# Kernel optimization log

Hardware: AMD Instinct MI355X
Metric: run time of the kernel (lower is better)

The kernel has to match this reference:

```python
import jax, jax.numpy as jnp
import numpy as np

S, B, D = 2048, 16, 512  # seq_len, batch, dim_in (= value_dim)


def setup_inputs() -> dict:
    key = jax.random.key(0)
    k1, k2, k3 = jax.random.split(key, 3)
    seq = jax.random.normal(k1, (S, B, D), dtype=jnp.float32)
    # torch nn.Linear(dim_in, value_dim): weight [value_dim, dim_in], bias [value_dim]
    bound = 1.0 / np.sqrt(D)
    Wv = jax.random.uniform(k2, (D, D), minval=-bound, maxval=bound, dtype=jnp.float32)
    bv = jax.random.uniform(k3, (D,), minval=-bound, maxval=bound, dtype=jnp.float32)
    return {"seq": seq, "Wv": Wv, "bv": bv}


def reference(seq, Wv, bv):
    # seq: [S, B, D] -> seq_in: [B, S, D]
    seq_in = jnp.transpose(seq, (1, 0, 2))
    # value = tanh(Linear(seq_in)); query = value; keys = seq_in (raw input)
    value = jnp.tanh(jnp.einsum('bsd,vd->bsv', seq_in, Wv) + bv)  # [B, S, Dv]
    # unscaled score matrix value @ value^T -> [B, S, S]
    weights = jnp.einsum('bsv,btv->bst', value, value)
    weights = jax.nn.softmax(weights, axis=-1)
    out = jnp.einsum('bst,btd->bsd', weights, seq_in)  # [B, S, D]
    return jnp.transpose(out, (1, 0, 2))  # [S, B, D]
```

## Files before the change

kernel.cpp:

```cpp
#include <hip/hip_runtime.h>

#define S_LEN 2048
#define BATCH 16
#define DIM   512
#define KVB   64
#define NT    (S_LEN / KVB)

typedef __bf16 bf16x8 __attribute__((ext_vector_type(8)));
typedef float  f32x4  __attribute__((ext_vector_type(4)));
typedef float  f32x16 __attribute__((ext_vector_type(16)));
typedef unsigned int u32x4 __attribute__((ext_vector_type(4)));

static __device__ __forceinline__ unsigned short f2bf(float f) {
    __bf16 h = (__bf16)f;
    return __builtin_bit_cast(unsigned short, h);
}
static __device__ __forceinline__ bf16x8 ld_bf8(const unsigned short* p) {
    u32x4 v = *reinterpret_cast<const u32x4*>(p);
    return __builtin_bit_cast(bf16x8, v);
}
static __device__ __forceinline__ f32x4 mfma16(bf16x8 a, bf16x8 b, f32x4 c) {
    return __builtin_amdgcn_mfma_f32_16x16x32_bf16(a, b, c, 0, 0, 0);
}
static __device__ __forceinline__ f32x16 mfma32(bf16x8 a, bf16x8 b, f32x16 c) {
    return __builtin_amdgcn_mfma_f32_32x32x16_bf16(a, b, c, 0, 0, 0);
}
static __device__ __forceinline__ void gload16(const unsigned short* g, unsigned short* l) {
    __builtin_amdgcn_global_load_lds(
        (const __attribute__((address_space(1))) unsigned int*)g,
        (__attribute__((address_space(3))) unsigned int*)l, 16, 0, 0);
}
#define WAITV(N) do { asm volatile("s_waitcnt vmcnt(" #N ")" ::: "memory"); \
                      __builtin_amdgcn_sched_barrier(0); } while (0)
static __device__ __forceinline__ void waitlg0() {
    asm volatile("s_waitcnt lgkmcnt(0)" ::: "memory");
    __builtin_amdgcn_sched_barrier(0);
}

__global__ void pack_seq(const float* __restrict__ seq, unsigned short* __restrict__ seqb,
                         unsigned short* __restrict__ vt) {
    __shared__ float tile[32][33];
    int b  = blockIdx.z;
    int d0 = blockIdx.y * 32;
    int s0 = blockIdx.x * 32;
    int t  = threadIdx.x;
    {
        int sl = t >> 3, c4 = (t & 7) * 4;
        float4 v = *reinterpret_cast<const float4*>(
            seq + (size_t)(s0 + sl) * (BATCH * DIM) + (size_t)b * DIM + d0 + c4);
        tile[sl][c4 + 0] = v.x; tile[sl][c4 + 1] = v.y;
        tile[sl][c4 + 2] = v.z; tile[sl][c4 + 3] = v.w;
        uint2 r;
        r.x = (unsigned)f2bf(v.x) | ((unsigned)f2bf(v.y) << 16);
        r.y = (unsigned)f2bf(v.z) | ((unsigned)f2bf(v.w) << 16);
        int s = s0 + sl, d = d0 + c4;
        size_t off = ((size_t)(b * 128 + (s >> 4)) * 16 + (d >> 5)) * 512
                     + (s & 15) * 32 + (d & 31);
        *reinterpret_cast<uint2*>(seqb + off) = r;
    }
    __syncthreads();
    {
        int dl = t >> 3, s4 = (t & 7) * 4;
        uint2 r;
        r.x = (unsigned)f2bf(tile[s4 + 0][dl]) | ((unsigned)f2bf(tile[s4 + 1][dl]) << 16);
        r.y = (unsigned)f2bf(tile[s4 + 2][dl]) | ((unsigned)f2bf(tile[s4 + 3][dl]) << 16);
        int d = d0 + dl, s = s0 + s4;
        size_t off = ((size_t)(b * 128 + (s >> 4)) * 16 + (d >> 5)) * 512
                     + (d & 31) * 16 + (s & 15);
        *reinterpret_cast<uint2*>(vt + off) = r;
    }
}

__global__ void pack_vt(const float* __restrict__ seq, unsigned short* __restrict__ vt) {
    __shared__ float tile[32][33];
    int b  = blockIdx.z;
    int d0 = blockIdx.y * 32;
    int s0 = blockIdx.x * 32;
    int t  = threadIdx.x;
    {
        int sl = t >> 3, c4 = (t & 7) * 4;
        float4 v = *reinterpret_cast<const float4*>(
            seq + (size_t)(s0 + sl) * (BATCH * DIM) + (size_t)b * DIM + d0 + c4);
        tile[sl][c4 + 0] = v.x; tile[sl][c4 + 1] = v.y;
        tile[sl][c4 + 2] = v.z; tile[sl][c4 + 3] = v.w;
    }
    __syncthreads();
    {
        int dl = t >> 3, s4 = (t & 7) * 4;
        uint2 r;
        r.x = (unsigned)f2bf(tile[s4 + 0][dl]) | ((unsigned)f2bf(tile[s4 + 1][dl]) << 16);
        r.y = (unsigned)f2bf(tile[s4 + 2][dl]) | ((unsigned)f2bf(tile[s4 + 3][dl]) << 16);
        int d = d0 + dl, s = s0 + s4;
        size_t off = ((size_t)(b * 128 + (s >> 4)) * 16 + (d >> 5)) * 512
                     + (d & 31) * 16 + (s & 15);
        *reinterpret_cast<uint2*>(vt + off) = r;
    }
}

template <bool BF16A>
__global__ void __launch_bounds__(256) gemm_value(
        const float* __restrict__ seq, const unsigned short* __restrict__ seqb,
        const float* __restrict__ wv, const float* __restrict__ bv,
        unsigned short* __restrict__ val) {
    __shared__ unsigned short Asm[64][72];
    __shared__ unsigned short Bsm[64][72];
    int t  = threadIdx.x;
    int rb = blockIdx.x * 64;
    int cb = blockIdx.y * 64;
    int w = t >> 6, l = t & 63;
    int mi = w >> 1, ni = w & 1;
    int l15 = l & 15, lh = l >> 4;
    f32x4 acc[2][2] = {};

    int srow = t >> 2;
    int qc   = (t & 3) * 16;
    int gr = rb + srow;
    int sb = gr >> 11, ss = gr & 2047;
    const float* aSrc = seq + ((size_t)ss * BATCH + sb) * DIM + qc;
    const float* bSrc = wv + (size_t)(cb + srow) * DIM + qc;

    for (int k0 = 0; k0 < DIM; k0 += 64) {
        if (BF16A) {
            int dcol = k0 + qc;
            const unsigned short* p = seqb
                + ((size_t)(sb * 128 + (ss >> 4)) * 16 + (dcol >> 5)) * 512
                + (ss & 15) * 32 + (dcol & 31);
            *reinterpret_cast<u32x4*>(&Asm[srow][qc])     = *reinterpret_cast<const u32x4*>(p);
            *reinterpret_cast<u32x4*>(&Asm[srow][qc + 8]) = *reinterpret_cast<const u32x4*>(p + 8);
        } else {
            unsigned short ar[16];
            #pragma unroll
            for (int j = 0; j < 4; ++j) {
                float4 v = *reinterpret_cast<const float4*>(aSrc + k0 + j * 4);
                ar[j * 4 + 0] = f2bf(v.x); ar[j * 4 + 1] = f2bf(v.y);
                ar[j * 4 + 2] = f2bf(v.z); ar[j * 4 + 3] = f2bf(v.w);
            }
            *reinterpret_cast<u32x4*>(&Asm[srow][qc])     = *reinterpret_cast<u32x4*>(&ar[0]);
            *reinterpret_cast<u32x4*>(&Asm[srow][qc + 8]) = *reinterpret_cast<u32x4*>(&ar[8]);
        }
        {
            unsigned short br[16];
            #pragma unroll
            for (int j = 0; j < 4; ++j) {
                float4 u = *reinterpret_cast<const float4*>(bSrc + k0 + j * 4);
                br[j * 4 + 0] = f2bf(u.x); br[j * 4 + 1] = f2bf(u.y);
                br[j * 4 + 2] = f2bf(u.z); br[j * 4 + 3] = f2bf(u.w);
            }
            *reinterpret_cast<u32x4*>(&Bsm[srow][qc])     = *reinterpret_cast<u32x4*>(&br[0]);
            *reinterpret_cast<u32x4*>(&Bsm[srow][qc + 8]) = *reinterpret_cast<u32x4*>(&br[8]);
        }
        __syncthreads();
        #pragma unroll
        for (int kf = 0; kf < 2; ++kf) {
            bf16x8 af[2], bfm[2];
            #pragma unroll
            for (int i = 0; i < 2; ++i)
                af[i] = ld_bf8(&Asm[mi * 32 + i * 16 + l15][kf * 32 + lh * 8]);
            #pragma unroll
            for (int j = 0; j < 2; ++j)
                bfm[j] = ld_bf8(&Bsm[ni * 32 + j * 16 + l15][kf * 32 + lh * 8]);
            #pragma unroll
            for (int i = 0; i < 2; ++i)
                #pragma unroll
                for (int j = 0; j < 2; ++j)
                    acc[i][j] = mfma16(af[i], bfm[j], acc[i][j]);
        }
        __syncthreads();
    }
    #pragma unroll
    for (int i = 0; i < 2; ++i) {
        #pragma unroll
        for (int j = 0; j < 2; ++j) {
            int gcol = cb + ni * 32 + j * 16 + l15;
            float bias = bv[gcol];
            #pragma unroll
            for (int r = 0; r < 4; ++r) {
                int grow = rb + mi * 32 + i * 16 + lh * 4 + r;
                float x = acc[i][j][r] + bias;
                int b_ = grow >> 11, s_ = grow & 2047;
                size_t off = ((size_t)(b_ * 128 + (s_ >> 4)) * 16 + (gcol >> 5)) * 512
                             + (s_ & 15) * 32 + (gcol & 31);
                val[off] = f2bf(tanhf(x));
            }
        }
    }
}

__global__ void __launch_bounds__(512, 2) attn_fused(
        const unsigned short* __restrict__ val, const unsigned short* __restrict__ vt,
        float* __restrict__ out) {
    extern __shared__ char smem[];
    unsigned short* Kb = (unsigned short*)smem;
    unsigned short* Vb = (unsigned short*)(smem + 65536);
    float*          Sb = (float*)(smem + 131072);
    unsigned short* PS = (unsigned short*)(smem + 148480);
    float* stm = (float*)(smem + 156928);
    float* stl = stm + 64;
    float* sts = stm + 128;

    const int t = threadIdx.x;
    const int w = t >> 6, l = t & 63;
    const int l15 = l & 15, lh = l >> 4;
    const int l31 = l & 31, lh1 = l >> 5;

    int wg  = blockIdx.x;
    int swz = (wg & 7) * 64 + (wg >> 3);
    int b   = swz >> 5;
    int qb  = (swz & 31) * 64;

    const int qi = w & 3, khi = w >> 2;
    const int dq = w;

    const unsigned short* valb = val + (size_t)b * 128 * 16 * 512;
    const unsigned short* vtb  = vt  + (size_t)b * 128 * 16 * 512;

    if (t < 64) { stm[t] = -3.0e38f; stl[t] = 0.0f; }

    bf16x8 qf[16];
    {
        const unsigned short* qp = valb + ((size_t)((qb >> 4) + qi) * 16) * 512
                                   + l15 * 32 + lh * 8;
        #pragma unroll
        for (int ks = 0; ks < 16; ++ks) qf[ks] = ld_bf8(qp + (size_t)ks * 512);
    }
    f32x16 o[4] = {};

    auto dmaK = [&](int kt) {
        #pragma unroll
        for (int i = 0; i < 8; ++i) {
            int idx = i * 8 + w, g = idx >> 4, ks = idx & 15;
            gload16(valb + ((size_t)(kt * 4 + g) * 16 + ks) * 512 + l15 * 32 + lh * 8,
                    Kb + idx * 512);
        }
    };
    auto dmaV = [&](int kt) {
        #pragma unroll
        for (int i = 0; i < 8; ++i) {
            int idx = i * 8 + w, ks = idx >> 4, dt = idx & 15;
            gload16(vtb + ((size_t)(kt * 4 + ks) * 16 + dt) * 512 + l31 * 16 + lh1 * 8,
                    Vb + idx * 512);
        }
    };

    dmaK(0);
    dmaV(0);
    WAITV(0);
    __builtin_amdgcn_s_barrier();

    for (int kt = 0; kt < NT; ++kt) {
        WAITV(8);
        __builtin_amdgcn_s_barrier();
        {
            const unsigned short* kb0 = Kb + (size_t)(2 * khi) * 16 * 512 + l * 8;
            const unsigned short* kb1 = kb0 + 16 * 512;
            f32x4 a0 = {}, a1 = {};
            __builtin_amdgcn_s_setprio(1);
            #pragma unroll
            for (int ks = 0; ks < 16; ++ks) {
                bf16x8 k0 = ld_bf8(kb0 + ks * 512);
                bf16x8 k1 = ld_bf8(kb1 + ks * 512);
                a0 = mfma16(qf[ks], k0, a0);
                a1 = mfma16(qf[ks], k1, a1);
            }
            __builtin_amdgcn_s_setprio(0);
            #pragma unroll
            for (int r = 0; r < 4; ++r) {
                Sb[(qi * 16 + lh * 4 + r) * 68 + khi * 32 + l15]      = a0[r];
                Sb[(qi * 16 + lh * 4 + r) * 68 + khi * 32 + 16 + l15] = a1[r];
            }
        }
        waitlg0();
        __builtin_amdgcn_s_barrier();

        {
            int nk = (kt + 1 < NT) ? kt + 1 : NT - 1;
            dmaK(nk);
        }
        {
            int row = t >> 3, e = t & 7;
            const float* sp = Sb + row * 68 + e * 8;
            f32x4 x0 = *reinterpret_cast<const f32x4*>(sp);
            f32x4 x1 = *reinterpret_cast<const f32x4*>(sp + 4);
            float mt = fmaxf(fmaxf(fmaxf(x0[0], x0[1]), fmaxf(x0[2], x0[3])),
                             fmaxf(fmaxf(x1[0], x1[1]), fmaxf(x1[2], x1[3])));
            #pragma unroll
            for (int m = 1; m <= 4; m <<= 1) mt = fmaxf(mt, __shfl_xor(mt, m, 64));
            float m_old = stm[row];
            float m_new = (mt > m_old + 8.0f) ? mt : m_old;
            float e0 = __expf(x0[0] - m_new), e1 = __expf(x0[1] - m_new);
            float e2 = __expf(x0[2] - m_new), e3 = __expf(x0[3] - m_new);
            float e4 = __expf(x1[0] - m_new), e5 = __expf(x1[1] - m_new);
            float e6 = __expf(x1[2] - m_new), e7 = __expf(x1[3] - m_new);
            float lt = ((e0 + e1) + (e2 + e3)) + ((e4 + e5) + (e6 + e7));
            #pragma unroll
            for (int m = 1; m <= 4; m <<= 1) lt += __shfl_xor(lt, m, 64);
            u32x4 pk;
            pk[0] = (unsigned)f2bf(e0) | ((unsigned)f2bf(e1) << 16);
            pk[1] = (unsigned)f2bf(e2) | ((unsigned)f2bf(e3) << 16);
            pk[2] = (unsigned)f2bf(e4) | ((unsigned)f2bf(e5) << 16);
            pk[3] = (unsigned)f2bf(e6) | ((unsigned)f2bf(e7) << 16);
            int ks = e >> 1, qg = row >> 5;
            unsigned short* pdst = PS + ((qg * 4 + ks) * 512 + ks * 8)
                                   + ((e & 1) * 32 + (row & 31)) * 8;
            *reinterpret_cast<u32x4*>(pdst) = pk;
            if (e == 0) {
                float alpha = (m_new == m_old) ? 1.0f : __expf(m_old - m_new);
                sts[row] = alpha;
                stm[row] = m_new;
                stl[row] = stl[row] * alpha + lt;
            }
        }
        waitlg0();
        WAITV(8);
        __builtin_amdgcn_s_barrier();

        {
            f32x4 al[2][4];
            bool need = false;
            #pragma unroll
            for (int qg = 0; qg < 2; ++qg)
                #pragma unroll
                for (int c = 0; c < 4; ++c) {
                    al[qg][c] = *reinterpret_cast<const f32x4*>(
                        sts + qg * 32 + 4 * lh1 + 8 * c);
                    #pragma unroll
                    for (int j = 0; j < 4; ++j) need = need || (al[qg][c][j] != 1.0f);
                }
            if (__any((int)need)) {
                #pragma unroll
                for (int qg = 0; qg < 2; ++qg)
                    #pragma unroll
                    for (int dtl = 0; dtl < 2; ++dtl)
                        #pragma unroll
                        for (int rr = 0; rr < 16; ++rr)
                            o[qg * 2 + dtl][rr] *= al[qg][rr >> 2][rr & 3];
            }
            __builtin_amdgcn_s_setprio(1);
            #pragma unroll
            for (int ks = 0; ks < 4; ++ks) {
                bf16x8 pa0 = ld_bf8(PS + ((0 + ks) * 512 + ks * 8) + l * 8);
                bf16x8 pa1 = ld_bf8(PS + ((4 + ks) * 512 + ks * 8) + l * 8);
                #pragma unroll
                for (int dtl = 0; dtl < 2; ++dtl) {
                    bf16x8 vf = ld_bf8(Vb + (size_t)(ks * 16 + dq * 2 + dtl) * 512 + l * 8);
                    o[0 + dtl] = mfma32(pa0, vf, o[0 + dtl]);
                    o[2 + dtl] = mfma32(pa1, vf, o[2 + dtl]);
                }
            }
            __builtin_amdgcn_s_setprio(0);
        }
        waitlg0();
        __builtin_amdgcn_s_barrier();
        {
            int nv = (kt + 1 < NT) ? kt + 1 : NT - 1;
            dmaV(nv);
        }
    }

    #pragma unroll
    for (int qg = 0; qg < 2; ++qg) {
        f32x4 li[4];
        #pragma unroll
        for (int c = 0; c < 4; ++c) {
            f32x4 lv = *reinterpret_cast<const f32x4*>(stl + qg * 32 + 4 * lh1 + 8 * c);
            #pragma unroll
            for (int j = 0; j < 4; ++j) li[c][j] = 1.0f / lv[j];
        }
        #pragma unroll
        for (int dtl = 0; dtl < 2; ++dtl) {
            int col = dq * 64 + dtl * 32 + l31;
            #pragma unroll
            for (int rr = 0; rr < 16; ++rr) {
                int cr  = (rr & 3) + 8 * (rr >> 2) + 4 * lh1;
                int row = qb + qg * 32 + cr;
                out[(size_t)row * (BATCH * DIM) + (size_t)b * DIM + col] =
                    o[qg * 2 + dtl][rr] * li[rr >> 2][rr & 3];
            }
        }
    }
}

extern "C" void kernel_launch(void* const* d_in, const int* in_sizes, int n_in,
                              void* d_out, int out_size, void* d_ws, size_t ws_size,
                              hipStream_t stream) {
    const float* seq = (const float*)d_in[0];
    const float* wv  = (const float*)d_in[1];
    const float* bv  = (const float*)d_in[2];
    float* outp = (float*)d_out;

    unsigned short* wsVal  = (unsigned short*)d_ws;
    unsigned short* wsVt   = (unsigned short*)((char*)d_ws + 33554432);
    unsigned short* wsSeqb = (unsigned short*)((char*)d_ws + 67108864);

    bool fused = ws_size >= 100663296ull;
    if (fused) {
        pack_seq<<<dim3(S_LEN / 32, DIM / 32, BATCH), dim3(256), 0, stream>>>(
            seq, wsSeqb, wsVt);
        gemm_value<true><<<dim3(BATCH * S_LEN / 64, DIM / 64), dim3(256), 0, stream>>>(
            seq, wsSeqb, wv, bv, wsVal);
    } else {
        pack_vt<<<dim3(S_LEN / 32, DIM / 32, BATCH), dim3(256), 0, stream>>>(seq, wsVt);
        gemm_value<false><<<dim3(BATCH * S_LEN / 64, DIM / 64), dim3(256), 0, stream>>>(
            seq, nullptr, wv, bv, wsVal);
    }
    attn_fused<<<dim3(512), dim3(512), 157696, stream>>>(wsVal, wsVt, outp);
}
```

Baseline: 296.5 us.

## Store tanh value tensor as FP8 e4m3 and compute QK scores with FP8 MFMA

The value projection output is now written as FP8 e4m3 in a repacked layout instead of bf16. The attention kernel computes scores with 16x16x32 fp8 MFMAs, using two accumulators per tile that are summed afterwards. This halves K/Q bytes loaded and LDS space for K, and the wait count is adjusted for fewer K DMA instructions. The cost is precision: unscaled scores summed over 512 dims feed a softmax, so FP8 rounding of tanh values may shift the attention weights noticeably.

```diff
diff --git a/kernel.cpp b/kernel.cpp
--- a/kernel.cpp
+++ b/kernel.cpp
@@ -1,4 +1,5 @@
 #include <hip/hip_runtime.h>
+#include <hip/hip_fp8.h>
 
 #define S_LEN 2048
 #define BATCH 16
@@ -10,11 +11,16 @@
 typedef float  f32x4  __attribute__((ext_vector_type(4)));
 typedef float  f32x16 __attribute__((ext_vector_type(16)));
 typedef unsigned int u32x4 __attribute__((ext_vector_type(4)));
+typedef long long llx2 __attribute__((ext_vector_type(2)));
 
 static __device__ __forceinline__ unsigned short f2bf(float f) {
     __bf16 h = (__bf16)f;
     return __builtin_bit_cast(unsigned short, h);
 }
+static __device__ __forceinline__ unsigned char f2fp8(float f) {
+    __hip_fp8_e4m3 h(f);
+    return h.__x;
+}
 static __device__ __forceinline__ bf16x8 ld_bf8(const unsigned short* p) {
     u32x4 v = *reinterpret_cast<const u32x4*>(p);
     return __builtin_bit_cast(bf16x8, v);
@@ -22,10 +28,13 @@
 static __device__ __forceinline__ f32x4 mfma16(bf16x8 a, bf16x8 b, f32x4 c) {
     return __builtin_amdgcn_mfma_f32_16x16x32_bf16(a, b, c, 0, 0, 0);
 }
+static __device__ __forceinline__ f32x4 mfma8(long long a, long long b, f32x4 c) {
+    return __builtin_amdgcn_mfma_f32_16x16x32_fp8_fp8(a, b, c, 0, 0, 0);
+}
 static __device__ __forceinline__ f32x16 mfma32(bf16x8 a, bf16x8 b, f32x16 c) {
     return __builtin_amdgcn_mfma_f32_32x32x16_bf16(a, b, c, 0, 0, 0);
 }
-static __device__ __forceinline__ void gload16(const unsigned short* g, unsigned short* l) {
+static __device__ __forceinline__ void gload16(const void* g, void* l) {
     __builtin_amdgcn_global_load_lds(
         (const __attribute__((address_space(1))) unsigned int*)g,
         (__attribute__((address_space(3))) unsigned int*)l, 16, 0, 0);
@@ -101,7 +110,7 @@
 __global__ void __launch_bounds__(256) gemm_value(
         const float* __restrict__ seq, const unsigned short* __restrict__ seqb,
         const float* __restrict__ wv, const float* __restrict__ bv,
-        unsigned short* __restrict__ val) {
+        unsigned char* __restrict__ val8) {
     __shared__ unsigned short Asm[64][72];
     __shared__ unsigned short Bsm[64][72];
     int t  = threadIdx.x;
@@ -173,28 +182,30 @@
         for (int j = 0; j < 2; ++j) {
             int gcol = cb + ni * 32 + j * 16 + l15;
             float bias = bv[gcol];
+            int kp = gcol & 63;
+            int p  = ((kp & 31) >> 3) * 16 + (kp >> 5) * 8 + (kp & 7);
             #pragma unroll
             for (int r = 0; r < 4; ++r) {
                 int grow = rb + mi * 32 + i * 16 + lh * 4 + r;
                 float x = acc[i][j][r] + bias;
                 int b_ = grow >> 11, s_ = grow & 2047;
-                size_t off = ((size_t)(b_ * 128 + (s_ >> 4)) * 16 + (gcol >> 5)) * 512
-                             + (s_ & 15) * 32 + (gcol & 31);
-                val[off] = f2bf(tanhf(x));
+                size_t off = ((size_t)(b_ * 128 + (s_ >> 4)) * 8 + (gcol >> 6)) * 1024
+                             + (s_ & 15) * 64 + p;
+                val8[off] = f2fp8(tanhf(x));
             }
         }
     }
 }
 
 __global__ void __launch_bounds__(512, 2) attn_fused(
-        const unsigned short* __restrict__ val, const unsigned short* __restrict__ vt,
+        const unsigned char* __restrict__ val8, const unsigned short* __restrict__ vt,
         float* __restrict__ out) {
     extern __shared__ char smem[];
-    unsigned short* Kb = (unsigned short*)smem;
-    unsigned short* Vb = (unsigned short*)(smem + 65536);
-    float*          Sb = (float*)(smem + 131072);
-    unsigned short* PS = (unsigned short*)(smem + 148480);
-    float* stm = (float*)(smem + 156928);
+    unsigned char*  Kb = (unsigned char*)smem;
+    unsigned short* Vb = (unsigned short*)(smem + 32768);
+    float*          Sb = (float*)(smem + 98304);
+    unsigned short* PS = (unsigned short*)(smem + 115712);
+    float* stm = (float*)(smem + 124160);
     float* stl = stm + 64;
     float* sts = stm + 128;
 
@@ -211,26 +222,30 @@
     const int qi = w & 3, khi = w >> 2;
     const int dq = w;
 
-    const unsigned short* valb = val + (size_t)b * 128 * 16 * 512;
-    const unsigned short* vtb  = vt  + (size_t)b * 128 * 16 * 512;
+    const unsigned char*  valb = val8 + (size_t)b * 128 * 8 * 1024;
+    const unsigned short* vtb  = vt   + (size_t)b * 128 * 16 * 512;
 
     if (t < 64) { stm[t] = -3.0e38f; stl[t] = 0.0f; }
 
-    bf16x8 qf[16];
+    long long qe[8], qo[8];
     {
-        const unsigned short* qp = valb + ((size_t)((qb >> 4) + qi) * 16) * 512
-                                   + l15 * 32 + lh * 8;
-        #pragma unroll
-        for (int ks = 0; ks < 16; ++ks) qf[ks] = ld_bf8(qp + (size_t)ks * 512);
+        const unsigned char* qp = valb + (size_t)((qb >> 4) + qi) * 8 * 1024
+                                  + l15 * 64 + lh * 16;
+        #pragma unroll
+        for (int s = 0; s < 8; ++s) {
+            u32x4 v = *reinterpret_cast<const u32x4*>(qp + s * 1024);
+            llx2 pr = __builtin_bit_cast(llx2, v);
+            qe[s] = pr[0]; qo[s] = pr[1];
+        }
     }
     f32x16 o[4] = {};
 
     auto dmaK = [&](int kt) {
         #pragma unroll
-        for (int i = 0; i < 8; ++i) {
-            int idx = i * 8 + w, g = idx >> 4, ks = idx & 15;
-            gload16(valb + ((size_t)(kt * 4 + g) * 16 + ks) * 512 + l15 * 32 + lh * 8,
-                    Kb + idx * 512);
+        for (int i = 0; i < 4; ++i) {
+            int idx = i * 8 + w, g = idx >> 3, s = idx & 7;
+            gload16(valb + ((size_t)(kt * 4 + g) * 8 + s) * 1024 + l15 * 64 + lh * 16,
+                    Kb + idx * 1024);
         }
     };
     auto dmaV = [&](int kt) {
@@ -251,22 +266,27 @@
         WAITV(8);
         __builtin_amdgcn_s_barrier();
         {
-            const unsigned short* kb0 = Kb + (size_t)(2 * khi) * 16 * 512 + l * 8;
-            const unsigned short* kb1 = kb0 + 16 * 512;
-            f32x4 a0 = {}, a1 = {};
+            const unsigned char* kb0 = Kb + (2 * khi) * 8192 + l * 16;
+            const unsigned char* kb1 = kb0 + 8192;
+            f32x4 a00 = {}, a01 = {}, a10 = {}, a11 = {};
             __builtin_amdgcn_s_setprio(1);
             #pragma unroll
-            for (int ks = 0; ks < 16; ++ks) {
-                bf16x8 k0 = ld_bf8(kb0 + ks * 512);
-                bf16x8 k1 = ld_bf8(kb1 + ks * 512);
-                a0 = mfma16(qf[ks], k0, a0);
-                a1 = mfma16(qf[ks], k1, a1);
+            for (int s = 0; s < 8; ++s) {
+                u32x4 k0 = *reinterpret_cast<const u32x4*>(kb0 + s * 1024);
+                u32x4 k1 = *reinterpret_cast<const u32x4*>(kb1 + s * 1024);
+                llx2 p0 = __builtin_bit_cast(llx2, k0);
+                llx2 p1 = __builtin_bit_cast(llx2, k1);
+                a00 = mfma8(qe[s], p0[0], a00);
+                a10 = mfma8(qe[s], p1[0], a10);
+                a01 = mfma8(qo[s], p0[1], a01);
+                a11 = mfma8(qo[s], p1[1], a11);
             }
             __builtin_amdgcn_s_setprio(0);
+            f32x4 s0 = a00 + a01, s1 = a10 + a11;
             #pragma unroll
             for (int r = 0; r < 4; ++r) {
-                Sb[(qi * 16 + lh * 4 + r) * 68 + khi * 32 + l15]      = a0[r];
-                Sb[(qi * 16 + lh * 4 + r) * 68 + khi * 32 + 16 + l15] = a1[r];
+                Sb[(qi * 16 + lh * 4 + r) * 68 + khi * 32 + l15]      = s0[r];
+                Sb[(qi * 16 + lh * 4 + r) * 68 + khi * 32 + 16 + l15] = s1[r];
             }
         }
         waitlg0();
@@ -311,7 +331,7 @@
             }
         }
         waitlg0();
-        WAITV(8);
+        WAITV(4);
         __builtin_amdgcn_s_barrier();
 
         {
@@ -388,7 +408,7 @@
     const float* bv  = (const float*)d_in[2];
     float* outp = (float*)d_out;
 
-    unsigned short* wsVal  = (unsigned short*)d_ws;
+    unsigned char*  wsVal8 = (unsigned char*)d_ws;
     unsigned short* wsVt   = (unsigned short*)((char*)d_ws + 33554432);
     unsigned short* wsSeqb = (unsigned short*)((char*)d_ws + 67108864);
 
@@ -397,11 +417,11 @@
         pack_seq<<<dim3(S_LEN / 32, DIM / 32, BATCH), dim3(256), 0, stream>>>(
             seq, wsSeqb, wsVt);
         gemm_value<true><<<dim3(BATCH * S_LEN / 64, DIM / 64), dim3(256), 0, stream>>>(
-            seq, wsSeqb, wv, bv, wsVal);
+            seq, wsSeqb, wv, bv, wsVal8);
     } else {
         pack_vt<<<dim3(S_LEN / 32, DIM / 32, BATCH), dim3(256), 0, stream>>>(seq, wsVt);
         gemm_value<false><<<dim3(BATCH * S_LEN / 64, DIM / 64), dim3(256), 0, stream>>>(
-            seq, nullptr, wv, bv, wsVal);
-    }
-    attn_fused<<<dim3(512), dim3(512), 157696, stream>>>(wsVal, wsVt, outp);
-}
+            seq, nullptr, wv, bv, wsVal8);
+    }
+    attn_fused<<<dim3(512), dim3(512), 124928, stream>>>(wsVal8, wsVt, outp);
+}
```

Result: faster. 268.6 us (-9.4%).
